# Kernel optimization log

Measured on AMD Instinct MI355X. Metric: run time of the kernel, lower is better.

The kernel has to match this reference:

```python
import jax, jax.numpy as jnp
import numpy as np

S, B, IN, HID, H, D, DFF, L, NC, EMB = 1024, 32, 3072, 256, 16, 16, 1024, 4, 1623, 10


def setup_inputs() -> dict:
    key = jax.random.key(0)
    ks = jax.random.split(key, 12)
    w = lambda k, shp: 0.02 * jax.random.normal(k, shp, dtype=jnp.float32)
    return {
        "x": jax.random.normal(ks[0], (S, B, IN), dtype=jnp.float32),
        "fb": jax.random.randint(ks[1], (S, B), 0, NC),
        "fc1_w": w(ks[2], (HID, IN)),
        "fc1_b": jnp.zeros((HID,), jnp.float32),
        "emb": w(ks[3], (NC, EMB)),
        "proj_w": w(ks[4], (HID, HID + EMB)),
        "proj_b": jnp.zeros((HID,), jnp.float32),
        "ln1_g": jnp.ones((L, HID), jnp.float32),
        "ln1_b": jnp.zeros((L, HID), jnp.float32),
        "slow_w": w(ks[5], (L, H * (3 * D + 1), HID)),
        "out_w": w(ks[6], (L, HID, H * D)),
        "ln2_g": jnp.ones((L, HID), jnp.float32),
        "ln2_b": jnp.zeros((L, HID), jnp.float32),
        "ff1_w": w(ks[7], (L, DFF, HID)),
        "ff1_b": jnp.zeros((L, DFF), jnp.float32),
        "ff2_w": w(ks[8], (L, HID, DFF)),
        "ff2_b": jnp.zeros((L, HID), jnp.float32),
        "outl_w": w(ks[9], (NC, HID)),
        "outl_b": jnp.zeros((NC,), jnp.float32),
    }


def _ln(x, g, b):
    m = jnp.mean(x, -1, keepdims=True)
    v = jnp.mean(jnp.square(x - m), -1, keepdims=True)
    return (x - m) * jax.lax.rsqrt(v + 1e-5) * g + b


def _delta_attn(x, g, b, sw, ow):
    # x: (S, B, HID); delta-rule fast-weight linear attention
    s, bsz, _ = x.shape
    qkvb = jnp.einsum('sbi,oi->sbo', _ln(x, g, b), sw).reshape(s, bsz, H, 3 * D + 1)
    q, k, v, beta = jnp.split(qkvb, [D, 2 * D, 3 * D], axis=-1)
    q = jax.nn.softmax(q, axis=-1)      # sum-normalized feature map
    k = jax.nn.softmax(k, axis=-1)
    beta = jax.nn.sigmoid(beta)         # (S,B,H,1)

    def step(W, inp):
        qt, kt, vt, bt = inp            # (B,H,D),(B,H,D),(B,H,D),(B,H,1)
        v_old = jnp.einsum('bhkv,bhk->bhv', W, kt)
        v_new = bt * vt + (1.0 - bt) * v_old
        W = W + jnp.einsum('bhk,bhv->bhkv', kt, v_new - v_old)
        return W, jnp.einsum('bhkv,bhk->bhv', W, qt)

    W0 = jnp.zeros((bsz, H, D, D), x.dtype)
    _, o = jax.lax.scan(step, W0, (q, k, v, beta))   # o: (S,B,H,D)
    return x + jnp.einsum('sbi,oi->sbo', o.reshape(s, bsz, H * D), ow)


def _ffn(x, g, b, w1, b1, w2, b2):
    h = jax.nn.relu(jnp.einsum('sbi,oi->sbo', _ln(x, g, b), w1) + b1)
    return x + jnp.einsum('sbi,oi->sbo', h, w2) + b2


def reference(x, fb, fc1_w, fc1_b, emb, proj_w, proj_b, ln1_g, ln1_b, slow_w,
              out_w, ln2_g, ln2_b, ff1_w, ff1_b, ff2_w, ff2_b, outl_w, outl_b):
    h = jnp.einsum('sbi,oi->sbo', x, fc1_w) + fc1_b
    h = jnp.concatenate([h, emb[fb]], axis=-1)
    h = jnp.einsum('sbi,oi->sbo', h, proj_w) + proj_b
    for l in range(L):
        h = _delta_attn(h, ln1_g[l], ln1_b[l], slow_w[l], out_w[l])
        h = _ffn(h, ln2_g[l], ln2_b[l], ff1_w[l], ff1_b[l], ff2_w[l], ff2_b[l])
    return jnp.einsum('sbi,oi->sbo', h, outl_w) + outl_b
```

## Files before the change

### kernel.cpp

```cpp
#include <hip/hip_runtime.h>
#include <hip/hip_bf16.h>

#define S_LEN  1024
#define B_SZ   32
#define IN_DIM 3072
#define HID    256
#define NHEAD  16
#define HDIM   16
#define DFF    1024
#define NLAYER 4
#define NCLS   1623
#define EMB_D  10
#define MROWS  (S_LEN * B_SZ)
#define QROW   56

using bf16   = __hip_bfloat16;
using short8 = __attribute__((ext_vector_type(8))) short;
using f32x4  = __attribute__((ext_vector_type(4))) float;

#define GLOAD16(g, l) __builtin_amdgcn_global_load_lds(                        \
    (const __attribute__((address_space(1))) void*)(g),                        \
    (__attribute__((address_space(3))) void*)(l), 16, 0, 0)

__device__ __forceinline__ float b2f(short s) {
    union { float f; unsigned u; } x;
    x.u = ((unsigned)(unsigned short)s) << 16;
    return x.f;
}

template<int FLAGS>
__global__ __launch_bounds__(256) void mgemm(
    const bf16* __restrict__ A, const bf16* __restrict__ W,
    const float* __restrict__ bias, void* C, int N, int K, int Wld)
{
    __shared__ bf16 sA[2][128 * 32];
    __shared__ bf16 sB[2][128 * 32];
    const int t    = threadIdx.x;
    const int lane = t & 63;
    const int wid  = t >> 6;
    const int wr   = wid >> 1, wc = wid & 1;
    const long bm  = (long)blockIdx.x * 128;
    const int  bn  = blockIdx.y * 128;
    const int  fr  = lane & 15;
    const int  fg  = lane >> 4;
    const int  row0 = t >> 2;
    const int  kq0  = (t & 3) << 3;

    f32x4 acc[4][4];
#pragma unroll
    for (int m = 0; m < 4; ++m)
#pragma unroll
        for (int n = 0; n < 4; ++n)
#pragma unroll
            for (int r = 0; r < 4; ++r) acc[m][n][r] = 0.f;

    const int nkt = K >> 5;

    auto stage = [&](int buf, int kt) {
        const int k0 = kt << 5;
        GLOAD16(A + (bm + row0)      * (long)K   + k0 + kq0, &sA[buf][(t      ) * 8]);
        GLOAD16(A + (bm + row0 + 64) * (long)K   + k0 + kq0, &sA[buf][(t + 256) * 8]);
        GLOAD16(W + (long)(bn + row0)      * Wld + k0 + kq0, &sB[buf][(t      ) * 8]);
        GLOAD16(W + (long)(bn + row0 + 64) * Wld + k0 + kq0, &sB[buf][(t + 256) * 8]);
    };

    stage(0, 0);
    __syncthreads();
    for (int kt = 0; kt < nkt; ++kt) {
        const int cur = kt & 1;
        if (kt + 1 < nkt) stage(cur ^ 1, kt + 1);
        short8 af[4], bg[4];
#pragma unroll
        for (int m = 0; m < 4; ++m)
            af[m] = *(const short8*)&sA[cur][(wr * 64 + m * 16 + fr) * 32 + fg * 8];
#pragma unroll
        for (int n = 0; n < 4; ++n)
            bg[n] = *(const short8*)&sB[cur][(wc * 64 + n * 16 + fr) * 32 + fg * 8];
#pragma unroll
        for (int m = 0; m < 4; ++m)
#pragma unroll
            for (int n = 0; n < 4; ++n)
                acc[m][n] = __builtin_amdgcn_mfma_f32_16x16x32_bf16(
                    af[m], bg[n], acc[m][n], 0, 0, 0);
        __syncthreads();
    }

    float bs[4];
#pragma unroll
    for (int n = 0; n < 4; ++n) {
        const int c = bn + wc * 64 + n * 16 + fr;
        bs[n] = ((FLAGS & 1) && c < N) ? bias[c] : 0.f;
    }
#pragma unroll
    for (int m = 0; m < 4; ++m) {
#pragma unroll
        for (int n = 0; n < 4; ++n) {
            const int c = bn + wc * 64 + n * 16 + fr;
            if (c < N) {
#pragma unroll
                for (int r = 0; r < 4; ++r) {
                    const long rw = bm + wr * 64 + m * 16 + fg * 4 + r;
                    float v = acc[m][n][r] + bs[n];
                    if (FLAGS & 2) v = fmaxf(v, 0.f);
                    if (FLAGS & 16) {
                        const int s = (int)(rw >> 5), b = (int)(rw & 31);
                        const int hh = c / 49, cc = c - hh * 49;
                        if (cc == 48) v = 1.f / (1.f + __expf(-v));
                        ((bf16*)C)[((long)(b * 16 + hh) * 1024 + s) * QROW + cc] =
                            __float2bfloat16(v);
                    } else if (FLAGS & 8) {
                        ((bf16*)C)[rw * N + c] = __float2bfloat16(v);
                    } else {
                        ((float*)C)[rw * N + c] = v;
                    }
                }
            }
        }
    }
}

template<int FLAGS>
__global__ __launch_bounds__(256) void gemm_ln(
    const bf16* __restrict__ A, const bf16* __restrict__ W,
    const float* __restrict__ bias, const float* __restrict__ lg,
    const float* __restrict__ lb, float* H, bf16* __restrict__ Y, int K)
{
    __shared__ bf16 sA[2][64 * 32];
    __shared__ bf16 sB[2][256 * 32];
    __shared__ float rsum[64][4];
    __shared__ float rsq[64][4];
    const int t    = threadIdx.x;
    const int lane = t & 63;
    const int w    = t >> 6;
    const int fr   = lane & 15;
    const int fg   = lane >> 4;
    const long bm  = (long)blockIdx.x * 64;

    f32x4 acc[4][4];
#pragma unroll
    for (int m = 0; m < 4; ++m)
#pragma unroll
        for (int n = 0; n < 4; ++n)
#pragma unroll
            for (int r = 0; r < 4; ++r) acc[m][n][r] = 0.f;

    const int nkt = K >> 5;
    auto stage = [&](int buf, int kt) {
        const int k0 = kt << 5;
        GLOAD16(A + (bm + (t >> 2)) * (long)K + k0 + ((t & 3) << 3),
                &sA[buf][t * 8]);
#pragma unroll
        for (int i = 0; i < 4; ++i)
            GLOAD16(W + (long)((i << 6) + (t >> 2)) * K + k0 + ((t & 3) << 3),
                    &sB[buf][(i * 256 + t) * 8]);
    };

    stage(0, 0);
    __syncthreads();
    for (int kt = 0; kt < nkt; ++kt) {
        const int cur = kt & 1;
        if (kt + 1 < nkt) stage(cur ^ 1, kt + 1);
        short8 af[4], bg[4];
#pragma unroll
        for (int m = 0; m < 4; ++m)
            af[m] = *(const short8*)&sA[cur][(m * 16 + fr) * 32 + fg * 8];
#pragma unroll
        for (int n = 0; n < 4; ++n)
            bg[n] = *(const short8*)&sB[cur][(w * 64 + n * 16 + fr) * 32 + fg * 8];
#pragma unroll
        for (int m = 0; m < 4; ++m)
#pragma unroll
            for (int n = 0; n < 4; ++n)
                acc[m][n] = __builtin_amdgcn_mfma_f32_16x16x32_bf16(
                    af[m], bg[n], acc[m][n], 0, 0, 0);
        __syncthreads();
    }

    float bs[4];
#pragma unroll
    for (int n = 0; n < 4; ++n) {
        const int c = w * 64 + n * 16 + fr;
        bs[n] = (FLAGS & 1) ? bias[c] : 0.f;
    }
    float ps[4][4], pq[4][4];
#pragma unroll
    for (int m = 0; m < 4; ++m)
#pragma unroll
        for (int r = 0; r < 4; ++r) { ps[m][r] = 0.f; pq[m][r] = 0.f; }
#pragma unroll
    for (int m = 0; m < 4; ++m)
#pragma unroll
        for (int n = 0; n < 4; ++n)
#pragma unroll
            for (int r = 0; r < 4; ++r) {
                const long rw = bm + m * 16 + fg * 4 + r;
                const int c = w * 64 + n * 16 + fr;
                float v = acc[m][n][r] + bs[n];
                if (FLAGS & 4) v += H[rw * HID + c];
                H[rw * HID + c] = v;
                acc[m][n][r] = v;
                ps[m][r] += v;
                pq[m][r] += v * v;
            }
    if (FLAGS & 8) {
#pragma unroll
        for (int m = 0; m < 4; ++m)
#pragma unroll
            for (int n = 0; n < 4; ++n)
#pragma unroll
                for (int r = 0; r < 4; ++r) {
                    const long rw = bm + m * 16 + fg * 4 + r;
                    const int c = w * 64 + n * 16 + fr;
                    Y[rw * HID + c] = __float2bfloat16(acc[m][n][r]);
                }
    } else {
#pragma unroll
        for (int m = 0; m < 4; ++m)
#pragma unroll
            for (int r = 0; r < 4; ++r) {
                float s = ps[m][r], q = pq[m][r];
                s += __shfl_xor(s, 1); q += __shfl_xor(q, 1);
                s += __shfl_xor(s, 2); q += __shfl_xor(q, 2);
                s += __shfl_xor(s, 4); q += __shfl_xor(q, 4);
                s += __shfl_xor(s, 8); q += __shfl_xor(q, 8);
                ps[m][r] = s; pq[m][r] = q;
            }
        if (fr == 0) {
#pragma unroll
            for (int m = 0; m < 4; ++m)
#pragma unroll
                for (int r = 0; r < 4; ++r) {
                    const int row = m * 16 + fg * 4 + r;
                    rsum[row][w] = ps[m][r];
                    rsq[row][w]  = pq[m][r];
                }
        }
        __syncthreads();
#pragma unroll
        for (int m = 0; m < 4; ++m)
#pragma unroll
            for (int r = 0; r < 4; ++r) {
                const int row = m * 16 + fg * 4 + r;
                const float4 s4 = *(const float4*)&rsum[row][0];
                const float4 q4 = *(const float4*)&rsq[row][0];
                const float S = (s4.x + s4.y) + (s4.z + s4.w);
                const float Q = (q4.x + q4.y) + (q4.z + q4.w);
                const float mean = S * (1.f / 256.f);
                const float inv  = rsqrtf(Q * (1.f / 256.f) - mean * mean + 1e-5f);
                const long rw = bm + row;
#pragma unroll
                for (int n = 0; n < 4; ++n) {
                    const int c = w * 64 + n * 16 + fr;
                    const float y = (acc[m][n][r] - mean) * inv * lg[c] + lb[c];
                    Y[rw * HID + c] = __float2bfloat16(y);
                }
            }
    }
}

__global__ __launch_bounds__(256) void fc1_k(
    const float* __restrict__ A, const bf16* __restrict__ W,
    const float* __restrict__ bias, bf16* __restrict__ hcat)
{
    __shared__ bf16 sA[2][128 * 32];
    __shared__ bf16 sB[2][128 * 32];
    const int t    = threadIdx.x;
    const int lane = t & 63;
    const int wid  = t >> 6;
    const int wr   = wid >> 1, wc = wid & 1;
    const long bm  = (long)blockIdx.x * 128;
    const int  bn  = blockIdx.y * 128;
    const int  fr  = lane & 15;
    const int  fg  = lane >> 4;
    const int  row0 = t >> 2;
    const int  kq0  = (t & 3) << 3;
    const int  arow = t >> 3;
    const int  ac4  = (t & 7) << 2;

    f32x4 acc[4][4];
#pragma unroll
    for (int m = 0; m < 4; ++m)
#pragma unroll
        for (int n = 0; n < 4; ++n)
#pragma unroll
            for (int r = 0; r < 4; ++r) acc[m][n][r] = 0.f;

    auto stageB = [&](int buf, int kt) {
        const int k0 = kt << 5;
        GLOAD16(W + (long)(bn + row0)      * IN_DIM + k0 + kq0, &sB[buf][(t      ) * 8]);
        GLOAD16(W + (long)(bn + row0 + 64) * IN_DIM + k0 + kq0, &sB[buf][(t + 256) * 8]);
    };
    float4 va[4];
    auto loadA = [&](int kt) {
        const int k0 = kt << 5;
#pragma unroll
        for (int rep = 0; rep < 4; ++rep)
            va[rep] = *(const float4*)(A + (bm + arow + rep * 32) * (long)IN_DIM + k0 + ac4);
    };
    auto writeA = [&](int buf) {
#pragma unroll
        for (int rep = 0; rep < 4; ++rep) {
            alignas(8) bf16 tb[4];
            tb[0] = __float2bfloat16(va[rep].x);
            tb[1] = __float2bfloat16(va[rep].y);
            tb[2] = __float2bfloat16(va[rep].z);
            tb[3] = __float2bfloat16(va[rep].w);
            *(ushort4*)&sA[buf][(arow + rep * 32) * 32 + ac4] = *(const ushort4*)tb;
        }
    };

    loadA(0);
    stageB(0, 0);
    writeA(0);
    __syncthreads();
    const int nkt = IN_DIM >> 5;
    for (int kt = 0; kt < nkt; ++kt) {
        const int cur = kt & 1;
        if (kt + 1 < nkt) { stageB(cur ^ 1, kt + 1); loadA(kt + 1); }
        short8 af[4], bg[4];
#pragma unroll
        for (int m = 0; m < 4; ++m)
            af[m] = *(const short8*)&sA[cur][(wr * 64 + m * 16 + fr) * 32 + fg * 8];
#pragma unroll
        for (int n = 0; n < 4; ++n)
            bg[n] = *(const short8*)&sB[cur][(wc * 64 + n * 16 + fr) * 32 + fg * 8];
#pragma unroll
        for (int m = 0; m < 4; ++m)
#pragma unroll
            for (int n = 0; n < 4; ++n)
                acc[m][n] = __builtin_amdgcn_mfma_f32_16x16x32_bf16(
                    af[m], bg[n], acc[m][n], 0, 0, 0);
        if (kt + 1 < nkt) writeA(cur ^ 1);
        __syncthreads();
    }

#pragma unroll
    for (int n = 0; n < 4; ++n) {
        const int c = bn + wc * 64 + n * 16 + fr;
        const float bsn = bias[c];
#pragma unroll
        for (int m = 0; m < 4; ++m)
#pragma unroll
            for (int r = 0; r < 4; ++r) {
                const long rw = bm + wr * 64 + m * 16 + fg * 4 + r;
                hcat[rw * 288 + c] = __float2bfloat16(acc[m][n][r] + bsn);
            }
    }
}

__global__ __launch_bounds__(256) void fillemb(
    const float* __restrict__ emb, const int* __restrict__ fb,
    bf16* __restrict__ hcat)
{
    const long row = (long)blockIdx.x * 8 + (threadIdx.x >> 5);
    const int c = threadIdx.x & 31;
    bf16 v = (c < EMB_D) ? __float2bfloat16(emb[(long)fb[row] * EMB_D + c])
                         : __float2bfloat16(0.f);
    hcat[row * 288 + 256 + c] = v;
}

__global__ __launch_bounds__(256) void cvtall(
    const float* __restrict__ fc1_w, const float* __restrict__ proj_w,
    const float* __restrict__ slow_w, const float* __restrict__ out_w,
    const float* __restrict__ ff1_w, const float* __restrict__ ff2_w,
    const float* __restrict__ outl_w, bf16* __restrict__ dst)
{
    for (long i = (long)blockIdx.x * 256 + threadIdx.x; i < 4562944L;
         i += (long)gridDim.x * 256) {
        float v;
        if (i < 786432L) {
            v = fc1_w[i];
        } else if (i < 860160L) {
            const long j = i - 786432L;
            const int r = (int)(j / 288), c = (int)(j - (long)r * 288);
            v = (c < 266) ? proj_w[(long)r * 266 + c] : 0.f;
        } else if (i < 1777664L) {
            const long j = i - 860160L;
            const int l = (int)(j / 229376);
            const long m = j - (long)l * 229376;
            const int r = (int)(m >> 8), c = (int)(m & 255);
            v = (r < 784) ? slow_w[(long)l * 200704 + (long)r * 256 + c] : 0.f;
        } else if (i < 2039808L) {
            v = out_w[i - 1777664L];
        } else if (i < 3088384L) {
            v = ff1_w[i - 2039808L];
        } else if (i < 4136960L) {
            v = ff2_w[i - 3088384L];
        } else {
            const long j = i - 4136960L;
            const int r = (int)(j >> 8), c = (int)(j & 255);
            v = (r < 1623) ? outl_w[(long)r * 256 + c] : 0.f;
        }
        dst[i] = __float2bfloat16(v);
    }
}

#define DOT16(dst, kr, s0, s1, s2, s3) do {                                    \
    float _pa = fmaf(kr[3],  (s0).w, fmaf(kr[2],  (s0).z, fmaf(kr[1],  (s0).y, kr[0]  * (s0).x))); \
    float _pb = fmaf(kr[7],  (s1).w, fmaf(kr[6],  (s1).z, fmaf(kr[5],  (s1).y, kr[4]  * (s1).x))); \
    float _pc = fmaf(kr[11], (s2).w, fmaf(kr[10], (s2).z, fmaf(kr[9],  (s2).y, kr[8]  * (s2).x))); \
    float _pd = fmaf(kr[15], (s3).w, fmaf(kr[14], (s3).z, fmaf(kr[13], (s3).y, kr[12] * (s3).x))); \
    dst = (_pa + _pb) + (_pc + _pd);                                           \
} while (0)

__global__ __launch_bounds__(64) void scan10(
    const bf16* __restrict__ qkvb, bf16* __restrict__ o)
{
    __shared__ short sbf[2][2048];
    __shared__ float wrk[32 * 52];
    __shared__ float W0l[16 * 20];
    __shared__ float DVl[16 * 20];
    const int lane = threadIdx.x;
    const int i4 = lane >> 2;
    const int jq = lane & 3;
    const int chain = blockIdx.x;
    const int b = chain >> 4, hh = chain & 15;
    const char* cbb = (const char*)(qkvb + (long)chain * S_LEN * QROW);
    bf16* po = o + (long)b * HID + hh * HDIM + jq * 4;

    for (int z = lane; z < 320; z += 64) W0l[z] = 0.f;

    auto stage = [&](int buf, int nb2) {
#pragma unroll
        for (int iss = 0; iss < 4; ++iss) {
            const char* src = cbb + (long)nb2 * 3584 + (iss * 64 + lane) * 16;
            GLOAD16(src, &sbf[buf][(iss * 64 + lane) * 8]);
        }
    };

    stage(0, 0);
    asm volatile("s_waitcnt vmcnt(0)" ::: "memory");
    for (int nb = 0; nb < 32; ++nb) {
        const int buf = nb & 1;
        asm volatile("s_waitcnt vmcnt(2)" ::: "memory");
        if (nb + 1 < 32) stage(buf ^ 1, nb + 1);

        {
            const int row = lane >> 1, hf = lane & 1;
            const short* ps = &sbf[buf][row * QROW + hf * 16];
            const short8 r0 = *(const short8*)(ps);
            const short8 r1 = *(const short8*)(ps + 8);
            float f[16];
#pragma unroll
            for (int j = 0; j < 8; ++j) { f[j] = b2f(r0[j]); f[8 + j] = b2f(r1[j]); }
            float mx = f[0];
#pragma unroll
            for (int j = 1; j < 16; ++j) mx = fmaxf(mx, f[j]);
            float sum = 0.f;
#pragma unroll
            for (int j = 0; j < 16; ++j) { f[j] = __expf(f[j] - mx); sum += f[j]; }
            const float inv = 1.f / sum;
            float* pw = wrk + row * 52 + hf * 16;
#pragma unroll
            for (int j = 0; j < 16; ++j) pw[j] = f[j] * inv;
            const short8 rv = *(const short8*)(&sbf[buf][row * QROW + 32 + hf * 8]);
            float* pv = wrk + row * 52 + 32 + hf * 8;
#pragma unroll
            for (int j = 0; j < 8; ++j) pv[j] = b2f(rv[j]);
            if (hf == 0)
                wrk[row * 52 + 48] = b2f(sbf[buf][row * QROW + 48]);
        }
        asm volatile("s_waitcnt lgkmcnt(0)" ::: "memory");

#pragma unroll
        for (int t = 0; t < 2; ++t) {
            const float* rb = wrk + t * 16 * 52;
            const float* myrow = rb + i4 * 52;
            float ki[16], qi[16];
            {
                const float4 kA = *(const float4*)(myrow + 16);
                const float4 kB = *(const float4*)(myrow + 20);
                const float4 kC = *(const float4*)(myrow + 24);
                const float4 kD = *(const float4*)(myrow + 28);
                ki[0]=kA.x; ki[1]=kA.y; ki[2]=kA.z; ki[3]=kA.w;
                ki[4]=kB.x; ki[5]=kB.y; ki[6]=kB.z; ki[7]=kB.w;
                ki[8]=kC.x; ki[9]=kC.y; ki[10]=kC.z; ki[11]=kC.w;
                ki[12]=kD.x; ki[13]=kD.y; ki[14]=kD.z; ki[15]=kD.w;
                const float4 qA = *(const float4*)(myrow);
                const float4 qB = *(const float4*)(myrow + 4);
                const float4 qC = *(const float4*)(myrow + 8);
                const float4 qD = *(const float4*)(myrow + 12);
                qi[0]=qA.x; qi[1]=qA.y; qi[2]=qA.z; qi[3]=qA.w;
                qi[4]=qB.x; qi[5]=qB.y; qi[6]=qB.z; qi[7]=qB.w;
                qi[8]=qC.x; qi[9]=qC.y; qi[10]=qC.z; qi[11]=qC.w;
                qi[12]=qD.x; qi[13]=qD.y; qi[14]=qD.z; qi[15]=qD.w;
            }
            const float beta = myrow[48];
            float gcf[4], qkc[4];
#pragma unroll
            for (int m = 0; m < 4; ++m) {
                const int s = jq * 4 + m;
                const float* sr = rb + s * 52 + 16;
                const float4 s0 = *(const float4*)(sr);
                const float4 s1 = *(const float4*)(sr + 4);
                const float4 s2 = *(const float4*)(sr + 8);
                const float4 s3 = *(const float4*)(sr + 12);
                float g, qk;
                DOT16(g, ki, s0, s1, s2, s3);
                DOT16(qk, qi, s0, s1, s2, s3);
                gcf[m] = (s < i4)  ? -beta * g : 0.f;
                qkc[m] = (s <= i4) ? qk : 0.f;
            }
            float P0=0,P1=0,P2=0,P3=0, O0=0,O1=0,O2=0,O3=0;
#pragma unroll
            for (int x = 0; x < 16; ++x) {
                const float4 w = *(const float4*)&W0l[x * 20 + jq * 4];
                P0 = fmaf(ki[x], w.x, P0); P1 = fmaf(ki[x], w.y, P1);
                P2 = fmaf(ki[x], w.z, P2); P3 = fmaf(ki[x], w.w, P3);
                O0 = fmaf(qi[x], w.x, O0); O1 = fmaf(qi[x], w.y, O1);
                O2 = fmaf(qi[x], w.z, O2); O3 = fmaf(qi[x], w.w, O3);
            }
            const float4 vv = *(const float4*)(myrow + 32 + jq * 4);
            float d0 = beta * (vv.x - P0), d1 = beta * (vv.y - P1);
            float d2 = beta * (vv.z - P2), d3 = beta * (vv.w - P3);
#pragma unroll
            for (int s = 0; s < 15; ++s) {
                const float cf = __shfl(gcf[s & 3], i4 * 4 + (s >> 2));
                const float e0 = __shfl(d0, s * 4 + jq);
                const float e1 = __shfl(d1, s * 4 + jq);
                const float e2 = __shfl(d2, s * 4 + jq);
                const float e3 = __shfl(d3, s * 4 + jq);
                d0 = fmaf(cf, e0, d0); d1 = fmaf(cf, e1, d1);
                d2 = fmaf(cf, e2, d2); d3 = fmaf(cf, e3, d3);
            }
            f32x4 dvv; dvv[0]=d0; dvv[1]=d1; dvv[2]=d2; dvv[3]=d3;
            *(f32x4*)&DVl[i4 * 20 + jq * 4] = dvv;
            asm volatile("s_waitcnt lgkmcnt(0)" ::: "memory");
            float a0=0,a1=0,a2=0,a3=0;
#pragma unroll
            for (int s = 0; s < 16; ++s) {
                const float4 dvs = *(const float4*)&DVl[s * 20 + jq * 4];
                const float cqk = __shfl(qkc[s & 3], i4 * 4 + (s >> 2));
                O0 = fmaf(cqk, dvs.x, O0); O1 = fmaf(cqk, dvs.y, O1);
                O2 = fmaf(cqk, dvs.z, O2); O3 = fmaf(cqk, dvs.w, O3);
                const float kx = rb[s * 52 + 16 + i4];
                a0 = fmaf(kx, dvs.x, a0); a1 = fmaf(kx, dvs.y, a1);
                a2 = fmaf(kx, dvs.z, a2); a3 = fmaf(kx, dvs.w, a3);
            }
            {
                const int sg = nb * 32 + t * 16 + i4;
                alignas(8) bf16 tb[4];
                tb[0] = __float2bfloat16(O0); tb[1] = __float2bfloat16(O1);
                tb[2] = __float2bfloat16(O2); tb[3] = __float2bfloat16(O3);
                *(ushort4*)((unsigned short*)(po + (long)sg * (B_SZ * HID))) =
                    *(const ushort4*)tb;
            }
            {
                float4 w = *(const float4*)&W0l[i4 * 20 + jq * 4];
                w.x += a0; w.y += a1; w.z += a2; w.w += a3;
                *(float4*)&W0l[i4 * 20 + jq * 4] = w;
            }
            asm volatile("s_waitcnt lgkmcnt(0)" ::: "memory");
        }
    }
}

extern "C" void kernel_launch(void* const* d_in, const int* in_sizes, int n_in,
                              void* d_out, int out_size, void* d_ws, size_t ws_size,
                              hipStream_t stream)
{
    const float* x      = (const float*)d_in[0];
    const int*   fb     = (const int*)  d_in[1];
    const float* fc1_w  = (const float*)d_in[2];
    const float* fc1_b  = (const float*)d_in[3];
    const float* emb    = (const float*)d_in[4];
    const float* proj_w = (const float*)d_in[5];
    const float* proj_b = (const float*)d_in[6];
    const float* ln1_g  = (const float*)d_in[7];
    const float* ln1_b  = (const float*)d_in[8];
    const float* slow_w = (const float*)d_in[9];
    const float* out_w  = (const float*)d_in[10];
    const float* ln2_g  = (const float*)d_in[11];
    const float* ln2_b  = (const float*)d_in[12];
    const float* ff1_w  = (const float*)d_in[13];
    const float* ff1_b  = (const float*)d_in[14];
    const float* ff2_w  = (const float*)d_in[15];
    const float* ff2_b  = (const float*)d_in[16];
    const float* outl_w = (const float*)d_in[17];
    const float* outl_b = (const float*)d_in[18];

    char* wp = (char*)d_ws;
    float* h    = (float*)wp;                 wp += (size_t)MROWS * HID * 4;
    bf16*  abuf = (bf16*)wp;                  wp += (size_t)MROWS * HID * 2;
    bf16*  fc1b = (bf16*)wp;                  wp += (size_t)HID * IN_DIM * 2;
    bf16*  projb= (bf16*)wp;                  wp += (size_t)HID * 288 * 2;
    bf16*  slowb= (bf16*)wp;                  wp += (size_t)NLAYER * 896 * HID * 2;
    bf16*  outwb= (bf16*)wp;                  wp += (size_t)NLAYER * HID * HID * 2;
    bf16*  ff1b = (bf16*)wp;                  wp += (size_t)NLAYER * DFF * HID * 2;
    bf16*  ff2b = (bf16*)wp;                  wp += (size_t)NLAYER * HID * DFF * 2;
    bf16*  outlb= (bf16*)wp;                  wp += (size_t)1664 * HID * 2;

    bf16*  hcat = (bf16*)d_out;
    bf16*  qkvb = (bf16*)d_out;
    bf16*  hff  = (bf16*)d_out;

    const dim3 blk(256);

    cvtall<<<dim3(1024), blk, 0, stream>>>(fc1_w, proj_w, slow_w, out_w,
                                           ff1_w, ff2_w, outl_w, fc1b);

    fc1_k<<<dim3(256, 2), blk, 0, stream>>>(x, fc1b, fc1_b, hcat);
    fillemb<<<dim3(MROWS / 8), blk, 0, stream>>>(emb, fb, hcat);
    gemm_ln<1><<<dim3(512), blk, 0, stream>>>(hcat, projb, proj_b,
                                              ln1_g, ln1_b, h, abuf, 288);

    for (int l = 0; l < NLAYER; ++l) {
        mgemm<16><<<dim3(256, 7), blk, 0, stream>>>(abuf, slowb + (size_t)l * 896 * HID,
                                                    nullptr, qkvb, 784, HID, HID);
        scan10<<<dim3(B_SZ * NHEAD), dim3(64), 0, stream>>>(qkvb, abuf);
        gemm_ln<4><<<dim3(512), blk, 0, stream>>>(abuf, outwb + (size_t)l * HID * HID,
                                                  nullptr, ln2_g + l * HID,
                                                  ln2_b + l * HID, h, abuf, HID);
        mgemm<11><<<dim3(256, 8), blk, 0, stream>>>(abuf, ff1b + (size_t)l * DFF * HID,
                                                    ff1_b + l * DFF, hff, DFF, HID, HID);
        if (l + 1 < NLAYER)
            gemm_ln<5><<<dim3(512), blk, 0, stream>>>(hff, ff2b + (size_t)l * HID * DFF,
                                                      ff2_b + l * HID,
                                                      ln1_g + (l + 1) * HID,
                                                      ln1_b + (l + 1) * HID, h, abuf, DFF);
        else
            gemm_ln<13><<<dim3(512), blk, 0, stream>>>(hff, ff2b + (size_t)l * HID * DFF,
                                                       ff2_b + l * HID,
                                                       nullptr, nullptr, h, abuf, DFF);
    }
    mgemm<1><<<dim3(256, 13), blk, 0, stream>>>(abuf, outlb, outl_b, d_out,
                                                NCLS, HID, HID);
}
```

Measured before the change: 1.620 ms.

## Precompute chunkwise delta-rule coefficient matrices in a parallel kernel before the scan

Adds a highly parallel coef_k kernel that, for each 16-step chunk, computes the triangular solve of the delta-rule recurrence applied to the QK and K matrices and writes them to scratch memory. The sequential scan kernel then streams these coefficients in alongside the inputs and replaces its serial 15-step shuffle solve and dot-product work with plain FMAs. This moves latency-bound work off the 512-block critical scan onto 8192 blocks, in exchange for an extra kernel launch and extra global traffic for coefficient buffers stored in the output region.

```diff
diff --git a/kernel.cpp b/kernel.cpp
--- a/kernel.cpp
+++ b/kernel.cpp
@@ -403,13 +403,124 @@
     dst = (_pa + _pb) + (_pc + _pd);                                           \
 } while (0)
 
-__global__ __launch_bounds__(64) void scan10(
-    const bf16* __restrict__ qkvb, bf16* __restrict__ o)
+__global__ __launch_bounds__(256) void coef_k(
+    const bf16* __restrict__ qkvb, float* __restrict__ cfb)
+{
+    __shared__ float wrkc[4][16 * 52];
+    __shared__ float Gm[4][16 * 17];
+    __shared__ float Mql[4][16 * 17];
+    const int tid = threadIdx.x;
+    const int w = tid >> 6, lane = tid & 63;
+    const int cg = blockIdx.x * 4 + w;
+    const int chain = cg >> 6;
+    const int ck = cg & 63;
+    const bf16* rows = qkvb + ((long)chain * S_LEN + (long)ck * 16) * QROW;
+    float* wk = wrkc[w];
+    float* G  = Gm[w];
+    float* M  = Mql[w];
+
+    if (lane < 32) {
+        const int row = lane >> 1, hf = lane & 1;
+        const short* ps = (const short*)(rows + (long)row * QROW) + hf * 16;
+        const short8 r0 = *(const short8*)(ps);
+        const short8 r1 = *(const short8*)(ps + 8);
+        float f[16];
+#pragma unroll
+        for (int j = 0; j < 8; ++j) { f[j] = b2f(r0[j]); f[8 + j] = b2f(r1[j]); }
+        float mx = f[0];
+#pragma unroll
+        for (int j = 1; j < 16; ++j) mx = fmaxf(mx, f[j]);
+        float sum = 0.f;
+#pragma unroll
+        for (int j = 0; j < 16; ++j) { f[j] = __expf(f[j] - mx); sum += f[j]; }
+        const float inv = 1.f / sum;
+        float* pw = wk + row * 52 + hf * 16;
+#pragma unroll
+        for (int j = 0; j < 16; ++j) pw[j] = f[j] * inv;
+        if (hf == 0)
+            wk[row * 52 + 48] = b2f(((const short*)(rows + (long)row * QROW))[48]);
+    }
+    asm volatile("s_waitcnt lgkmcnt(0)" ::: "memory");
+
+    const int i4 = lane >> 2, jq = lane & 3;
+    {
+        const float* myrow = wk + i4 * 52;
+        float ki[16], qi[16];
+        const float4 kA = *(const float4*)(myrow + 16);
+        const float4 kB = *(const float4*)(myrow + 20);
+        const float4 kC = *(const float4*)(myrow + 24);
+        const float4 kD = *(const float4*)(myrow + 28);
+        ki[0]=kA.x; ki[1]=kA.y; ki[2]=kA.z; ki[3]=kA.w;
+        ki[4]=kB.x; ki[5]=kB.y; ki[6]=kB.z; ki[7]=kB.w;
+        ki[8]=kC.x; ki[9]=kC.y; ki[10]=kC.z; ki[11]=kC.w;
+        ki[12]=kD.x; ki[13]=kD.y; ki[14]=kD.z; ki[15]=kD.w;
+        const float4 qA = *(const float4*)(myrow);
+        const float4 qB = *(const float4*)(myrow + 4);
+        const float4 qC = *(const float4*)(myrow + 8);
+        const float4 qD = *(const float4*)(myrow + 12);
+        qi[0]=qA.x; qi[1]=qA.y; qi[2]=qA.z; qi[3]=qA.w;
+        qi[4]=qB.x; qi[5]=qB.y; qi[6]=qB.z; qi[7]=qB.w;
+        qi[8]=qC.x; qi[9]=qC.y; qi[10]=qC.z; qi[11]=qC.w;
+        qi[12]=qD.x; qi[13]=qD.y; qi[14]=qD.z; qi[15]=qD.w;
+        const float beta = myrow[48];
+#pragma unroll
+        for (int m = 0; m < 4; ++m) {
+            const int s = jq * 4 + m;
+            const float* sr = wk + s * 52 + 16;
+            const float4 s0 = *(const float4*)(sr);
+            const float4 s1 = *(const float4*)(sr + 4);
+            const float4 s2 = *(const float4*)(sr + 8);
+            const float4 s3 = *(const float4*)(sr + 12);
+            float g, qk;
+            DOT16(g, ki, s0, s1, s2, s3);
+            DOT16(qk, qi, s0, s1, s2, s3);
+            G[i4 * 17 + s] = (s < i4)  ? beta * g : 0.f;
+            M[i4 * 17 + s] = (s <= i4) ? qk : 0.f;
+        }
+    }
+    asm volatile("s_waitcnt lgkmcnt(0)" ::: "memory");
+
+    {
+        const int cs = i4, rq = jq;
+        float A1r[4], A2r[4];
+#pragma unroll
+        for (int j = 0; j < 4; ++j)
+            A1r[j] = M[(rq * 4 + j) * 17 + cs];
+        const float4 kcol = *(const float4*)&wk[cs * 52 + 16 + rq * 4];
+        A2r[0] = kcol.x; A2r[1] = kcol.y; A2r[2] = kcol.z; A2r[3] = kcol.w;
+#pragma unroll
+        for (int t = 15; t >= 1; --t) {
+            const float Lc = G[t * 17 + cs];
+            const float b10 = __shfl(A1r[0], t * 4 + rq);
+            const float b11 = __shfl(A1r[1], t * 4 + rq);
+            const float b12 = __shfl(A1r[2], t * 4 + rq);
+            const float b13 = __shfl(A1r[3], t * 4 + rq);
+            const float b20 = __shfl(A2r[0], t * 4 + rq);
+            const float b21 = __shfl(A2r[1], t * 4 + rq);
+            const float b22 = __shfl(A2r[2], t * 4 + rq);
+            const float b23 = __shfl(A2r[3], t * 4 + rq);
+            A1r[0] = fmaf(-Lc, b10, A1r[0]); A1r[1] = fmaf(-Lc, b11, A1r[1]);
+            A1r[2] = fmaf(-Lc, b12, A1r[2]); A1r[3] = fmaf(-Lc, b13, A1r[3]);
+            A2r[0] = fmaf(-Lc, b20, A2r[0]); A2r[1] = fmaf(-Lc, b21, A2r[1]);
+            A2r[2] = fmaf(-Lc, b22, A2r[2]); A2r[3] = fmaf(-Lc, b23, A2r[3]);
+        }
+        float* dst = cfb + (long)cg * 512;
+        f32x4 o1; o1[0]=A1r[0]; o1[1]=A1r[1]; o1[2]=A1r[2]; o1[3]=A1r[3];
+        f32x4 o2; o2[0]=A2r[0]; o2[1]=A2r[1]; o2[2]=A2r[2]; o2[3]=A2r[3];
+        *(f32x4*)(dst + cs * 16 + rq * 4) = o1;
+        *(f32x4*)(dst + 256 + cs * 16 + rq * 4) = o2;
+    }
+}
+
+__global__ __launch_bounds__(64) void scan11(
+    const bf16* __restrict__ qkvb, const float* __restrict__ cfb,
+    bf16* __restrict__ o)
 {
     __shared__ short sbf[2][2048];
+    __shared__ float scf[2][1024];
     __shared__ float wrk[32 * 52];
     __shared__ float W0l[16 * 20];
-    __shared__ float DVl[16 * 20];
+    __shared__ float EVl[16 * 20];
     const int lane = threadIdx.x;
     const int i4 = lane >> 2;
     const int jq = lane & 3;
@@ -426,6 +537,10 @@
             const char* src = cbb + (long)nb2 * 3584 + (iss * 64 + lane) * 16;
             GLOAD16(src, &sbf[buf][(iss * 64 + lane) * 8]);
         }
+        const float* csrc = cfb + ((long)chain * 64 + nb2 * 2) * 512;
+#pragma unroll
+        for (int iss = 0; iss < 4; ++iss)
+            GLOAD16(csrc + (iss * 64 + lane) * 4, &scf[buf][(iss * 64 + lane) * 4]);
     };
 
     stage(0, 0);
@@ -466,6 +581,12 @@
         for (int t = 0; t < 2; ++t) {
             const float* rb = wrk + t * 16 * 52;
             const float* myrow = rb + i4 * 52;
+            float QKTr[16], KT2r[16];
+#pragma unroll
+            for (int s = 0; s < 16; ++s) {
+                QKTr[s] = scf[buf][t * 512 + s * 16 + i4];
+                KT2r[s] = scf[buf][t * 512 + 256 + s * 16 + i4];
+            }
             float ki[16], qi[16];
             {
                 const float4 kA = *(const float4*)(myrow + 16);
@@ -486,21 +607,6 @@
                 qi[12]=qD.x; qi[13]=qD.y; qi[14]=qD.z; qi[15]=qD.w;
             }
             const float beta = myrow[48];
-            float gcf[4], qkc[4];
-#pragma unroll
-            for (int m = 0; m < 4; ++m) {
-                const int s = jq * 4 + m;
-                const float* sr = rb + s * 52 + 16;
-                const float4 s0 = *(const float4*)(sr);
-                const float4 s1 = *(const float4*)(sr + 4);
-                const float4 s2 = *(const float4*)(sr + 8);
-                const float4 s3 = *(const float4*)(sr + 12);
-                float g, qk;
-                DOT16(g, ki, s0, s1, s2, s3);
-                DOT16(qk, qi, s0, s1, s2, s3);
-                gcf[m] = (s < i4)  ? -beta * g : 0.f;
-                qkc[m] = (s <= i4) ? qk : 0.f;
-            }
             float P0=0,P1=0,P2=0,P3=0, O0=0,O1=0,O2=0,O3=0;
 #pragma unroll
             for (int x = 0; x < 16; ++x) {
@@ -511,31 +617,19 @@
                 O2 = fmaf(qi[x], w.z, O2); O3 = fmaf(qi[x], w.w, O3);
             }
             const float4 vv = *(const float4*)(myrow + 32 + jq * 4);
-            float d0 = beta * (vv.x - P0), d1 = beta * (vv.y - P1);
-            float d2 = beta * (vv.z - P2), d3 = beta * (vv.w - P3);
-#pragma unroll
-            for (int s = 0; s < 15; ++s) {
-                const float cf = __shfl(gcf[s & 3], i4 * 4 + (s >> 2));
-                const float e0 = __shfl(d0, s * 4 + jq);
-                const float e1 = __shfl(d1, s * 4 + jq);
-                const float e2 = __shfl(d2, s * 4 + jq);
-                const float e3 = __shfl(d3, s * 4 + jq);
-                d0 = fmaf(cf, e0, d0); d1 = fmaf(cf, e1, d1);
-                d2 = fmaf(cf, e2, d2); d3 = fmaf(cf, e3, d3);
-            }
-            f32x4 dvv; dvv[0]=d0; dvv[1]=d1; dvv[2]=d2; dvv[3]=d3;
-            *(f32x4*)&DVl[i4 * 20 + jq * 4] = dvv;
+            f32x4 ev;
+            ev[0] = beta * (vv.x - P0); ev[1] = beta * (vv.y - P1);
+            ev[2] = beta * (vv.z - P2); ev[3] = beta * (vv.w - P3);
+            *(f32x4*)&EVl[i4 * 20 + jq * 4] = ev;
             asm volatile("s_waitcnt lgkmcnt(0)" ::: "memory");
             float a0=0,a1=0,a2=0,a3=0;
 #pragma unroll
             for (int s = 0; s < 16; ++s) {
-                const float4 dvs = *(const float4*)&DVl[s * 20 + jq * 4];
-                const float cqk = __shfl(qkc[s & 3], i4 * 4 + (s >> 2));
-                O0 = fmaf(cqk, dvs.x, O0); O1 = fmaf(cqk, dvs.y, O1);
-                O2 = fmaf(cqk, dvs.z, O2); O3 = fmaf(cqk, dvs.w, O3);
-                const float kx = rb[s * 52 + 16 + i4];
-                a0 = fmaf(kx, dvs.x, a0); a1 = fmaf(kx, dvs.y, a1);
-                a2 = fmaf(kx, dvs.z, a2); a3 = fmaf(kx, dvs.w, a3);
+                const float4 es = *(const float4*)&EVl[s * 20 + jq * 4];
+                O0 = fmaf(QKTr[s], es.x, O0); O1 = fmaf(QKTr[s], es.y, O1);
+                O2 = fmaf(QKTr[s], es.z, O2); O3 = fmaf(QKTr[s], es.w, O3);
+                a0 = fmaf(KT2r[s], es.x, a0); a1 = fmaf(KT2r[s], es.y, a1);
+                a2 = fmaf(KT2r[s], es.z, a2); a3 = fmaf(KT2r[s], es.w, a3);
             }
             {
                 const int sg = nb * 32 + t * 16 + i4;
@@ -592,6 +686,7 @@
 
     bf16*  hcat = (bf16*)d_out;
     bf16*  qkvb = (bf16*)d_out;
+    float* cfb  = (float*)((bf16*)d_out + (size_t)512 * 1024 * QROW);
     bf16*  hff  = (bf16*)d_out;
 
     const dim3 blk(256);
@@ -607,7 +702,8 @@
     for (int l = 0; l < NLAYER; ++l) {
         mgemm<16><<<dim3(256, 7), blk, 0, stream>>>(abuf, slowb + (size_t)l * 896 * HID,
                                                     nullptr, qkvb, 784, HID, HID);
-        scan10<<<dim3(B_SZ * NHEAD), dim3(64), 0, stream>>>(qkvb, abuf);
+        coef_k<<<dim3(8192), blk, 0, stream>>>(qkvb, cfb);
+        scan11<<<dim3(B_SZ * NHEAD), dim3(64), 0, stream>>>(qkvb, cfb, abuf);
         gemm_ln<4><<<dim3(512), blk, 0, stream>>>(abuf, outwb + (size_t)l * HID * HID,
                                                   nullptr, ln2_g + l * HID,
                                                   ln2_b + l * HID, h, abuf, HID);
```

Measured after the change: 1.571 ms. 1.03x faster.
